# Performance work log

Measured on AMD Instinct MI355X. Metric: run time of the kernel, lower is better.

The kernel has to match this reference:

```python
import jax, jax.numpy as jnp
import numpy as np

D = 128
EMB = 1024
B, S = 4, 4096


def setup_inputs() -> dict:
    key = jax.random.key(0)
    ks = jax.random.split(key, 7)
    scale = 1.0 / np.sqrt(EMB)
    return {
        "X": jax.random.normal(ks[0], (B, S, EMB), dtype=jnp.float32),
        "lam": jnp.float32(0.8),
        "Wq": jax.random.uniform(ks[1], (EMB, 2 * D), jnp.float32, -scale, scale),
        "bq": jax.random.uniform(ks[2], (2 * D,), jnp.float32, -scale, scale),
        "Wk": jax.random.uniform(ks[3], (EMB, 2 * D), jnp.float32, -scale, scale),
        "bk": jax.random.uniform(ks[4], (2 * D,), jnp.float32, -scale, scale),
        "Wv": jax.random.uniform(ks[5], (EMB, D), jnp.float32, -scale, scale),
        "bv": jax.random.uniform(ks[6], (D,), jnp.float32, -scale, scale),
    }


def reference(X, lam, Wq, bq, Wk, bk, Wv, bv):
    # Projections: Q,K are [B,S,2d]; V is [B,S,d]
    Q = X @ Wq + bq
    K = X @ Wk + bk
    V = X @ Wv + bv
    Q1, Q2 = Q[..., :D], Q[..., D:]
    K1, K2 = K[..., :D], K[..., D:]
    s = 1.0 / jnp.sqrt(jnp.float32(D))
    # Dual QK^T scores [B,S,S]
    A1 = jnp.einsum("bqd,bkd->bqk", Q1, K1) * s
    A2 = jnp.einsum("bqd,bkd->bqk", Q2, K2) * s
    P = jax.nn.softmax(A1, axis=-1) - lam * jax.nn.softmax(A2, axis=-1)
    return jnp.einsum("bqk,bkd->bqd", P, V)
```

## Files before the change

### kernel.cpp

```cpp
#include <hip/hip_runtime.h>
#include <hip/hip_bf16.h>


typedef __attribute__((ext_vector_type(8))) short bf16x8;
typedef __attribute__((ext_vector_type(4))) float f32x4;
typedef __attribute__((ext_vector_type(16))) float f32x16;

#define MFMA16(a, b, c) __builtin_amdgcn_mfma_f32_16x16x32_bf16((a), (b), (c), 0, 0, 0)
#define MFMA32(a, b, c) __builtin_amdgcn_mfma_f32_32x32x16_bf16((a), (b), (c), 0, 0, 0)

__device__ __forceinline__ unsigned short f2bf(float x) {
    union { float f; unsigned u; } v; v.f = x;
    return (unsigned short)((v.u + 0x7FFFu + ((v.u >> 16) & 1u)) >> 16);
}
__device__ __forceinline__ unsigned pk2bf(float a, float b) {
    __hip_bfloat162 h = __float22bfloat162_rn(float2{a, b});
    union { __hip_bfloat162 h2; unsigned u; } cv; cv.h2 = h;
    return cv.u;
}
__device__ __forceinline__ float fexp2(float x) {
    float r; asm("v_exp_f32 %0, %1" : "=v"(r) : "v"(x)); return r;
}

__global__ __launch_bounds__(256) void wtrans_kernel(
    const float* __restrict__ Wq, const float* __restrict__ Wk,
    const float* __restrict__ Wv, unsigned short* __restrict__ Wt) {
    int tid = blockIdx.x * 256 + threadIdx.x;
    int k = tid & 1023, n = tid >> 10;
    float v;
    if (n < 256)      v = Wq[k * 256 + n];
    else if (n < 512) v = Wk[k * 256 + (n - 256)];
    else              v = Wv[k * 128 + (n - 512)];
    Wt[tid] = f2bf(v);
}

__global__ __launch_bounds__(256) void proj_kernel(
    const float* __restrict__ X, const unsigned short* __restrict__ Wt,
    const float* __restrict__ bq, const float* __restrict__ bk,
    const float* __restrict__ bv,
    unsigned short* __restrict__ Qs, unsigned short* __restrict__ Kb,
    unsigned short* __restrict__ Vb) {
    __shared__ alignas(16) char lds[16384];
    const int nt = blockIdx.y;
    const int m0 = blockIdx.x * 128;
    const int t = threadIdx.x, w = t >> 6, l = t & 63, c = l & 15, g = l >> 4;
    const int wm = w >> 1, wn = w & 1;
    const unsigned short* Wrow = Wt + (long)(nt * 128) * 1024;

    f32x4 acc[4][4];
    const f32x4 fz = {0.f, 0.f, 0.f, 0.f};
#pragma unroll
    for (int i = 0; i < 4; i++)
#pragma unroll
        for (int j = 0; j < 4; j++) acc[i][j] = fz;

    const int srow = t >> 1, sh = t & 1;
    const int sswz = (srow & 7) << 4;
    for (int k0 = 0; k0 < 1024; k0 += 32) {
        const float* xs = X + (long)(m0 + srow) * 1024 + k0 + sh * 16;
        float4 f0 = *(const float4*)(xs + 0);
        float4 f1 = *(const float4*)(xs + 4);
        float4 f2 = *(const float4*)(xs + 8);
        float4 f3 = *(const float4*)(xs + 12);
        const unsigned short* wsc = Wrow + (long)srow * 1024 + k0 + sh * 16;
        uint4 w0 = *(const uint4*)(wsc + 0);
        uint4 w1 = *(const uint4*)(wsc + 8);
        uint4 xa, xb;
        xa.x = pk2bf(f0.x, f0.y); xa.y = pk2bf(f0.z, f0.w);
        xa.z = pk2bf(f1.x, f1.y); xa.w = pk2bf(f1.z, f1.w);
        xb.x = pk2bf(f2.x, f2.y); xb.y = pk2bf(f2.z, f2.w);
        xb.z = pk2bf(f3.x, f3.y); xb.w = pk2bf(f3.z, f3.w);
        int base = srow * 64 + sh * 32;
        *(uint4*)(lds + ((base + 0) ^ sswz)) = xa;
        *(uint4*)(lds + ((base + 16) ^ sswz)) = xb;
        *(uint4*)(lds + 8192 + ((base + 0) ^ sswz)) = w0;
        *(uint4*)(lds + 8192 + ((base + 16) ^ sswz)) = w1;
        __syncthreads();

        bf16x8 af[4];
#pragma unroll
        for (int am = 0; am < 4; am++) {
            int r_ = wm * 64 + am * 16 + c;
            af[am] = *(const bf16x8*)(lds + ((r_ * 64 + g * 16) ^ ((c & 7) << 4)));
        }
#pragma unroll
        for (int bn = 0; bn < 4; bn++) {
            int r_ = wn * 64 + bn * 16 + c;
            bf16x8 bfr = *(const bf16x8*)(lds + 8192 + ((r_ * 64 + g * 16) ^ ((c & 7) << 4)));
#pragma unroll
            for (int am = 0; am < 4; am++) acc[am][bn] = MFMA16(af[am], bfr, acc[am][bn]);
        }
        __syncthreads();
    }

    const float QSCALE = 0.08838834764831845f * 1.4426950408889634f;
    const float* bias; float scale; unsigned short* outp; int ostride, ocol0, boff;
    if (nt < 2)      { bias = bq; boff = nt * 128;       scale = QSCALE; outp = Qs; ostride = 256; ocol0 = nt * 128; }
    else if (nt < 4) { bias = bk; boff = (nt - 2) * 128; scale = 1.0f;   outp = Kb; ostride = 256; ocol0 = (nt - 2) * 128; }
    else             { bias = bv; boff = 0;              scale = 1.0f;   outp = Vb; ostride = 128; ocol0 = 0; }
#pragma unroll
    for (int bn = 0; bn < 4; bn++) {
        int ncol = wn * 64 + bn * 16 + c;
        float bb = bias[boff + ncol];
#pragma unroll
        for (int am = 0; am < 4; am++) {
#pragma unroll
            for (int r = 0; r < 4; r++) {
                long row = m0 + wm * 64 + am * 16 + 4 * g + r;
                outp[row * ostride + ocol0 + ncol] = f2bf((acc[am][bn][r] + bb) * scale);
            }
        }
    }
}

__global__ __launch_bounds__(256) void vtrans_kernel(
    const unsigned short* __restrict__ Vb, unsigned short* __restrict__ Vt) {
    int tid = blockIdx.x * 256 + threadIdx.x;
    int s = tid & 4095, d = (tid >> 12) & 127, b = tid >> 19;
    Vt[tid] = Vb[(((long)b << 12) + s) * 128 + d];
}

__global__ __launch_bounds__(512) void attn2_kernel(
    const unsigned short* __restrict__ Qs, const unsigned short* __restrict__ Kb,
    const unsigned short* __restrict__ Vt,
    float* __restrict__ Po, float* __restrict__ Ps, int nsplit, int ks) {
    __shared__ alignas(16) char lds[49152];
    const int t = threadIdx.x;
    const int w = t >> 6, l = t & 63, r31 = l & 31, hi = l >> 5;
    const int wq = w >> 1, br = w & 1;

    const int total = gridDim.x;
    const int lin = (blockIdx.x & 7) * (total >> 3) + (blockIdx.x >> 3);
    const int grp = lin >> 5, qb = lin & 31;
    const int b = grp / nsplit, split = grp % nsplit;

    const long qrow = (long)b * 4096 + qb * 128 + wq * 32 + r31;
    bf16x8 qf[8];
    const unsigned short* Qp = Qs + qrow * 256 + br * 128 + hi * 8;
#pragma unroll
    for (int ds = 0; ds < 8; ds++) qf[ds] = *(const bf16x8*)(Qp + ds * 16);

    f32x16 o[4];
    const f32x16 oz = {};
#pragma unroll
    for (int dt = 0; dt < 4; dt++) o[dt] = oz;
    float m = -1e30f, s = 0.f;

    const int krow = t >> 4, kseg = t & 15, khalf = kseg >> 3;
    const int kdoff = khalf * 8192 + (((krow * 256 + (kseg & 7) * 32)) ^
                                      (((krow & 7) << 4) ^ (khalf << 5)));
    const int vrow = t >> 2, vq = t & 3;
    const unsigned short* vsrc = Vt + (((long)b * 128 + vrow) << 12);
    const int voff = 16384 + ((vrow * 64 + vq * 16) ^ ((vrow & 7) << 4));
    const long kbb = (long)b * 4096;

    const int kb0 = split * ks, kend = kb0 + ks;
    uint4 kr0, kr1, vr0;
#define LOADTILE(KN)                                                        \
    {                                                                       \
        const unsigned short* kp = Kb + (kbb + (KN) + krow) * 256 + kseg * 16; \
        kr0 = *(const uint4*)(kp);                                          \
        kr1 = *(const uint4*)(kp + 8);                                      \
        vr0 = *(const uint4*)(vsrc + (KN) + vq * 8);                        \
    }
#define WRITETILE(BUF)                                                      \
    {                                                                       \
        char* bb_ = lds + (BUF)*24576;                                      \
        *(uint4*)(bb_ + kdoff) = kr0;                                       \
        *(uint4*)(bb_ + (kdoff ^ 16)) = kr1;                                \
        *(uint4*)(bb_ + voff) = vr0;                                        \
    }

    LOADTILE(kb0);
    WRITETILE(0);
    {
        int kn = (kb0 + 32 < kend) ? kb0 + 32 : kb0;
        LOADTILE(kn);
    }

    const int krd_sw = ((r31 & 7) << 4) ^ (br << 5);
    const int kbofs = br * 8192;
    int cur = 0;

    for (int kb = kb0; kb < kend; kb += 32) {
        __syncthreads();
        if (kb + 32 < kend) {
            WRITETILE(cur ^ 1);
            int kn = (kb + 64 < kend) ? kb + 64 : kb0;
            LOADTILE(kn);
        }
        const char* bufp = lds + cur * 24576;
        const char* kbase = bufp + kbofs;

        f32x16 pa = oz, pb_ = oz;
#pragma unroll
        for (int ds = 0; ds < 4; ds++) {
            bf16x8 kfa = *(const bf16x8*)(kbase + ((r31 * 256 + ds * 32 + hi * 16) ^ krd_sw));
            bf16x8 kfb = *(const bf16x8*)(kbase + ((r31 * 256 + (ds + 4) * 32 + hi * 16) ^ krd_sw));
            pa = MFMA32(kfa, qf[ds], pa);
            pb_ = MFMA32(kfb, qf[ds + 4], pb_);
        }
        f32x16 p;
#pragma unroll
        for (int i = 0; i < 16; i++) p[i] = pa[i] + pb_[i];

        float x0 = fmaxf(fmaxf(p[0], p[1]), fmaxf(p[2], p[3]));
        float x1 = fmaxf(fmaxf(p[4], p[5]), fmaxf(p[6], p[7]));
        float x2 = fmaxf(fmaxf(p[8], p[9]), fmaxf(p[10], p[11]));
        float x3 = fmaxf(fmaxf(p[12], p[13]), fmaxf(p[14], p[15]));
        float lmx = fmaxf(fmaxf(x0, x1), fmaxf(x2, x3));
        lmx = fmaxf(lmx, __shfl_xor(lmx, 32));
        if (__any(lmx > m + 8.f)) {
            float mn = fmaxf(m, lmx);
            float al = fexp2(m - mn);
            s *= al; m = mn;
#pragma unroll
            for (int dt = 0; dt < 4; dt++) o[dt] *= al;
        }
        float pe[16];
#pragma unroll
        for (int i = 0; i < 16; i++) pe[i] = fexp2(p[i] - m);
        float s0 = (pe[0] + pe[1]) + (pe[2] + pe[3]);
        float s1 = (pe[4] + pe[5]) + (pe[6] + pe[7]);
        float s2 = (pe[8] + pe[9]) + (pe[10] + pe[11]);
        float s3 = (pe[12] + pe[13]) + (pe[14] + pe[15]);
        float ps_ = (s0 + s1) + (s2 + s3);
        ps_ += __shfl_xor(ps_, 32);
        s += ps_;

        unsigned cA = pk2bf(pe[0], pe[1]), cB = pk2bf(pe[2], pe[3]);
        unsigned cC = pk2bf(pe[4], pe[5]), cD = pk2bf(pe[6], pe[7]);
        asm volatile("v_permlane32_swap_b32 %0, %1" : "+v"(cA), "+v"(cC));
        asm volatile("v_permlane32_swap_b32 %0, %1" : "+v"(cB), "+v"(cD));
        unsigned dA = pk2bf(pe[8], pe[9]), dB = pk2bf(pe[10], pe[11]);
        unsigned dC = pk2bf(pe[12], pe[13]), dD = pk2bf(pe[14], pe[15]);
        asm volatile("v_permlane32_swap_b32 %0, %1" : "+v"(dA), "+v"(dC));
        asm volatile("v_permlane32_swap_b32 %0, %1" : "+v"(dB), "+v"(dD));
        union { uint4 u; bf16x8 v; } pb0, pb1;
        pb0.u = uint4{cA, cB, cC, cD};
        pb1.u = uint4{dA, dB, dC, dD};

#pragma unroll
        for (int dt = 0; dt < 4; dt++) {
            int vr = dt * 32 + r31;
            int vsw = (vr & 7) << 4;
            bf16x8 vf0 = *(const bf16x8*)(bufp + 16384 + ((vr * 64 + hi * 16) ^ vsw));
            bf16x8 vf1 = *(const bf16x8*)(bufp + 16384 + ((vr * 64 + 32 + hi * 16) ^ vsw));
            o[dt] = MFMA32(vf0, pb0.v, o[dt]);
            o[dt] = MFMA32(vf1, pb1.v, o[dt]);
        }
        cur ^= 1;
    }

    float* po = Po + (((qrow)*nsplit + split) * 2 + br) * 128;
#pragma unroll
    for (int dt = 0; dt < 4; dt++) {
#pragma unroll
        for (int rg = 0; rg < 4; rg++) {
            float4 v;
            v.x = o[dt][rg * 4 + 0];
            v.y = o[dt][rg * 4 + 1];
            v.z = o[dt][rg * 4 + 2];
            v.w = o[dt][rg * 4 + 3];
            *(float4*)(po + dt * 32 + rg * 8 + hi * 4) = v;
        }
    }
    if (hi == 0)
        *(float2*)(Ps + (qrow * nsplit + split) * 4 + br * 2) = float2{m, s};
}

__global__ __launch_bounds__(256) void combine_kernel(
    const float* __restrict__ Po, const float* __restrict__ Ps,
    const float* __restrict__ lam_p, float* __restrict__ out, int nsplit) {
    int tid = blockIdx.x * 256 + threadIdx.x;
    int q = tid >> 5, dq = (tid & 31) * 4;
    float M1 = -1e30f, M2 = -1e30f;
    for (int s = 0; s < nsplit; s++) {
        float4 st = *(const float4*)(Ps + (long)(q * nsplit + s) * 4);
        M1 = fmaxf(M1, st.x); M2 = fmaxf(M2, st.z);
    }
    float S1 = 0.f, S2 = 0.f;
    float a0 = 0.f, a1 = 0.f, a2 = 0.f, a3 = 0.f;
    float b0 = 0.f, b1 = 0.f, b2 = 0.f, b3 = 0.f;
    for (int s = 0; s < nsplit; s++) {
        float4 st = *(const float4*)(Ps + (long)(q * nsplit + s) * 4);
        float w1 = fexp2(st.x - M1), w2 = fexp2(st.z - M2);
        S1 += st.y * w1; S2 += st.w * w2;
        const float* p1 = Po + (((long)q * nsplit + s) * 2 + 0) * 128 + dq;
        const float* p2 = Po + (((long)q * nsplit + s) * 2 + 1) * 128 + dq;
        float4 v1 = *(const float4*)p1;
        float4 v2 = *(const float4*)p2;
        a0 += v1.x * w1; a1 += v1.y * w1; a2 += v1.z * w1; a3 += v1.w * w1;
        b0 += v2.x * w2; b1 += v2.y * w2; b2 += v2.z * w2; b3 += v2.w * w2;
    }
    float lam = *lam_p;
    float i1 = 1.f / S1, i2 = lam / S2;
    float4 v;
    v.x = a0 * i1 - b0 * i2;
    v.y = a1 * i1 - b1 * i2;
    v.z = a2 * i1 - b2 * i2;
    v.w = a3 * i1 - b3 * i2;
    *(float4*)(out + (long)q * 128 + dq) = v;
}

extern "C" void kernel_launch(void* const* d_in, const int* in_sizes, int n_in,
                              void* d_out, int out_size, void* d_ws, size_t ws_size,
                              hipStream_t stream) {
    const float* X   = (const float*)d_in[0];
    const float* lam = (const float*)d_in[1];
    const float* Wq  = (const float*)d_in[2];
    const float* bq  = (const float*)d_in[3];
    const float* Wk  = (const float*)d_in[4];
    const float* bk  = (const float*)d_in[5];
    const float* Wv  = (const float*)d_in[6];
    const float* bv  = (const float*)d_in[7];
    char* ws = (char*)d_ws;
    unsigned short* Qs = (unsigned short*)(ws);
    unsigned short* Kb = (unsigned short*)(ws + (8u << 20));
    unsigned short* Vb = (unsigned short*)(ws + (16u << 20));
    unsigned short* Vt = (unsigned short*)(ws + (20u << 20));
    unsigned short* Wt = (unsigned short*)(ws + (24u << 20));
    const size_t base = (size_t)26 << 20;
    const size_t NQ = 16384;
    int nsplit = 1;
    if (ws_size >= base + NQ * 4 * 2 * 128 * 4 + NQ * 4 * 4 * 4)      nsplit = 4;
    else if (ws_size >= base + NQ * 2 * 2 * 128 * 4 + NQ * 2 * 4 * 4) nsplit = 2;
    float* Po = (float*)(ws + base);
    float* Ps = (float*)(ws + base + NQ * (size_t)nsplit * 2 * 128 * 4);

    wtrans_kernel<<<2560, 256, 0, stream>>>(Wq, Wk, Wv, Wt);
    proj_kernel<<<dim3(128, 5), 256, 0, stream>>>(X, Wt, bq, bk, bv, Qs, Kb, Vb);
    vtrans_kernel<<<8192, 256, 0, stream>>>(Vb, Vt);
    attn2_kernel<<<128 * nsplit, 512, 0, stream>>>(Qs, Kb, Vt, Po, Ps,
                                                   nsplit, 4096 / nsplit);
    combine_kernel<<<2048, 256, 0, stream>>>(Po, Ps, lam, (float*)d_out, nsplit);
}
```

Before: 172.6 us.

## Fuse V transpose into projection epilogue and halve attention block size

The projection kernel now writes V directly in transposed layout, which removes the separate vtrans kernel launch and its global round-trip. The attention kernel moves from 512-thread, 128-query blocks to 256-thread, 64-query blocks with twice as many blocks. Each thread loads more per tile, LDS swizzles are replaced by precomputed rotation offsets, and s_setprio is raised around the MFMA sections. The V epilogue stores are strided scatter writes, and the smaller blocks reload K/V tiles more often per query.

```diff
diff --git a/kernel.cpp b/kernel.cpp
--- a/kernel.cpp
+++ b/kernel.cpp
@@ -39,7 +39,7 @@
     const float* __restrict__ bq, const float* __restrict__ bk,
     const float* __restrict__ bv,
     unsigned short* __restrict__ Qs, unsigned short* __restrict__ Kb,
-    unsigned short* __restrict__ Vb) {
+    unsigned short* __restrict__ Vt) {
     __shared__ alignas(16) char lds[16384];
     const int nt = blockIdx.y;
     const int m0 = blockIdx.x * 128;
@@ -94,33 +94,42 @@
     }
 
     const float QSCALE = 0.08838834764831845f * 1.4426950408889634f;
-    const float* bias; float scale; unsigned short* outp; int ostride, ocol0, boff;
-    if (nt < 2)      { bias = bq; boff = nt * 128;       scale = QSCALE; outp = Qs; ostride = 256; ocol0 = nt * 128; }
-    else if (nt < 4) { bias = bk; boff = (nt - 2) * 128; scale = 1.0f;   outp = Kb; ostride = 256; ocol0 = (nt - 2) * 128; }
-    else             { bias = bv; boff = 0;              scale = 1.0f;   outp = Vb; ostride = 128; ocol0 = 0; }
-#pragma unroll
-    for (int bn = 0; bn < 4; bn++) {
-        int ncol = wn * 64 + bn * 16 + c;
-        float bb = bias[boff + ncol];
-#pragma unroll
-        for (int am = 0; am < 4; am++) {
-#pragma unroll
-            for (int r = 0; r < 4; r++) {
-                long row = m0 + wm * 64 + am * 16 + 4 * g + r;
-                outp[row * ostride + ocol0 + ncol] = f2bf((acc[am][bn][r] + bb) * scale);
+    if (nt < 4) {
+        const float* bias; float scale; unsigned short* outp; int ocol0, boff;
+        if (nt < 2) { bias = bq; boff = nt * 128;       scale = QSCALE; outp = Qs; ocol0 = nt * 128; }
+        else        { bias = bk; boff = (nt - 2) * 128; scale = 1.0f;   outp = Kb; ocol0 = (nt - 2) * 128; }
+#pragma unroll
+        for (int bn = 0; bn < 4; bn++) {
+            int ncol = wn * 64 + bn * 16 + c;
+            float bb = bias[boff + ncol];
+#pragma unroll
+            for (int am = 0; am < 4; am++) {
+#pragma unroll
+                for (int r = 0; r < 4; r++) {
+                    long row = m0 + wm * 64 + am * 16 + 4 * g + r;
+                    outp[row * 256 + ocol0 + ncol] = f2bf((acc[am][bn][r] + bb) * scale);
+                }
             }
         }
-    }
-}
-
-__global__ __launch_bounds__(256) void vtrans_kernel(
-    const unsigned short* __restrict__ Vb, unsigned short* __restrict__ Vt) {
-    int tid = blockIdx.x * 256 + threadIdx.x;
-    int s = tid & 4095, d = (tid >> 12) & 127, b = tid >> 19;
-    Vt[tid] = Vb[(((long)b << 12) + s) * 128 + d];
-}
-
-__global__ __launch_bounds__(512) void attn2_kernel(
+    } else {
+#pragma unroll
+        for (int bn = 0; bn < 4; bn++) {
+            int ncol = wn * 64 + bn * 16 + c;
+            float bb = bv[ncol];
+            unsigned short* vcol = Vt + ((long)((m0 >> 12) * 128 + ncol) << 12);
+#pragma unroll
+            for (int am = 0; am < 4; am++) {
+#pragma unroll
+                for (int r = 0; r < 4; r++) {
+                    int ss = (m0 & 4095) + wm * 64 + am * 16 + 4 * g + r;
+                    vcol[ss] = f2bf(acc[am][bn][r] + bb);
+                }
+            }
+        }
+    }
+}
+
+__global__ __launch_bounds__(256) void attn2_kernel(
     const unsigned short* __restrict__ Qs, const unsigned short* __restrict__ Kb,
     const unsigned short* __restrict__ Vt,
     float* __restrict__ Po, float* __restrict__ Ps, int nsplit, int ks) {
@@ -131,10 +140,10 @@
 
     const int total = gridDim.x;
     const int lin = (blockIdx.x & 7) * (total >> 3) + (blockIdx.x >> 3);
-    const int grp = lin >> 5, qb = lin & 31;
+    const int grp = lin >> 6, qb = lin & 63;
     const int b = grp / nsplit, split = grp % nsplit;
 
-    const long qrow = (long)b * 4096 + qb * 128 + wq * 32 + r31;
+    const long qrow = (long)b * 4096 + qb * 64 + wq * 32 + r31;
     bf16x8 qf[8];
     const unsigned short* Qp = Qs + qrow * 256 + br * 128 + hi * 8;
 #pragma unroll
@@ -146,29 +155,54 @@
     for (int dt = 0; dt < 4; dt++) o[dt] = oz;
     float m = -1e30f, s = 0.f;
 
-    const int krow = t >> 4, kseg = t & 15, khalf = kseg >> 3;
-    const int kdoff = khalf * 8192 + (((krow * 256 + (kseg & 7) * 32)) ^
-                                      (((krow & 7) << 4) ^ (khalf << 5)));
-    const int vrow = t >> 2, vq = t & 3;
-    const unsigned short* vsrc = Vt + (((long)b * 128 + vrow) << 12);
-    const int voff = 16384 + ((vrow * 64 + vq * 16) ^ ((vrow & 7) << 4));
+    const int krow = t >> 3, kseg = t & 7;
+    const int khalf = kseg >> 2, kcb = (kseg & 3) * 64;
+    int kw[4];
+#pragma unroll
+    for (int j = 0; j < 4; j++)
+        kw[j] = khalf * 8192 + krow * 256 + ((kcb + j * 16 + (krow << 4)) & 255);
+    const int vrow = t >> 1, vhalf = t & 1;
+    int vw[2];
+#pragma unroll
+    for (int j = 0; j < 2; j++)
+        vw[j] = 16384 + vrow * 64 + ((vhalf * 32 + j * 16 + ((vrow >> 1) << 4)) & 63);
+    const unsigned short* vsrc = Vt + (((long)b * 128 + vrow) << 12) + vhalf * 16;
     const long kbb = (long)b * 4096;
 
     const int kb0 = split * ks, kend = kb0 + ks;
-    uint4 kr0, kr1, vr0;
-#define LOADTILE(KN)                                                        \
-    {                                                                       \
-        const unsigned short* kp = Kb + (kbb + (KN) + krow) * 256 + kseg * 16; \
-        kr0 = *(const uint4*)(kp);                                          \
-        kr1 = *(const uint4*)(kp + 8);                                      \
-        vr0 = *(const uint4*)(vsrc + (KN) + vq * 8);                        \
-    }
-#define WRITETILE(BUF)                                                      \
-    {                                                                       \
-        char* bb_ = lds + (BUF)*24576;                                      \
-        *(uint4*)(bb_ + kdoff) = kr0;                                       \
-        *(uint4*)(bb_ + (kdoff ^ 16)) = kr1;                                \
-        *(uint4*)(bb_ + voff) = vr0;                                        \
+    uint4 kA, kB, kC, kD, vA, vB;
+#define LOADTILE(KN)                                                           \
+    {                                                                          \
+        const unsigned short* kp = Kb + (kbb + (KN) + krow) * 256 + kseg * 32; \
+        kA = *(const uint4*)(kp);                                              \
+        kB = *(const uint4*)(kp + 8);                                          \
+        kC = *(const uint4*)(kp + 16);                                         \
+        kD = *(const uint4*)(kp + 24);                                         \
+        const unsigned short* vp = vsrc + (KN);                                \
+        vA = *(const uint4*)(vp);                                              \
+        vB = *(const uint4*)(vp + 8);                                          \
+    }
+#define WRITETILE(BUF)                                                         \
+    {                                                                          \
+        char* bb_ = lds + (BUF)*24576;                                         \
+        *(uint4*)(bb_ + kw[0]) = kA;                                           \
+        *(uint4*)(bb_ + kw[1]) = kB;                                           \
+        *(uint4*)(bb_ + kw[2]) = kC;                                           \
+        *(uint4*)(bb_ + kw[3]) = kD;                                           \
+        *(uint4*)(bb_ + vw[0]) = vA;                                           \
+        *(uint4*)(bb_ + vw[1]) = vB;                                           \
+    }
+
+    int kro[8];
+#pragma unroll
+    for (int ds = 0; ds < 8; ds++)
+        kro[ds] = br * 8192 + r31 * 256 + ((ds * 32 + hi * 16 + (r31 << 4)) & 255);
+    int vro0[4], vro1[4];
+#pragma unroll
+    for (int dt = 0; dt < 4; dt++) {
+        int vr = dt * 32 + r31;
+        vro0[dt] = 16384 + vr * 64 + ((hi * 16 + ((vr >> 1) << 4)) & 63);
+        vro1[dt] = 16384 + vr * 64 + ((32 + hi * 16 + ((vr >> 1) << 4)) & 63);
     }
 
     LOADTILE(kb0);
@@ -177,9 +211,6 @@
         int kn = (kb0 + 32 < kend) ? kb0 + 32 : kb0;
         LOADTILE(kn);
     }
-
-    const int krd_sw = ((r31 & 7) << 4) ^ (br << 5);
-    const int kbofs = br * 8192;
     int cur = 0;
 
     for (int kb = kb0; kb < kend; kb += 32) {
@@ -190,16 +221,17 @@
             LOADTILE(kn);
         }
         const char* bufp = lds + cur * 24576;
-        const char* kbase = bufp + kbofs;
 
         f32x16 pa = oz, pb_ = oz;
+        __builtin_amdgcn_s_setprio(1);
 #pragma unroll
         for (int ds = 0; ds < 4; ds++) {
-            bf16x8 kfa = *(const bf16x8*)(kbase + ((r31 * 256 + ds * 32 + hi * 16) ^ krd_sw));
-            bf16x8 kfb = *(const bf16x8*)(kbase + ((r31 * 256 + (ds + 4) * 32 + hi * 16) ^ krd_sw));
+            bf16x8 kfa = *(const bf16x8*)(bufp + kro[ds]);
+            bf16x8 kfb = *(const bf16x8*)(bufp + kro[ds + 4]);
             pa = MFMA32(kfa, qf[ds], pa);
             pb_ = MFMA32(kfb, qf[ds + 4], pb_);
         }
+        __builtin_amdgcn_s_setprio(0);
         f32x16 p;
 #pragma unroll
         for (int i = 0; i < 16; i++) p[i] = pa[i] + pb_[i];
@@ -240,19 +272,19 @@
         pb0.u = uint4{cA, cB, cC, cD};
         pb1.u = uint4{dA, dB, dC, dD};
 
+        __builtin_amdgcn_s_setprio(1);
 #pragma unroll
         for (int dt = 0; dt < 4; dt++) {
-            int vr = dt * 32 + r31;
-            int vsw = (vr & 7) << 4;
-            bf16x8 vf0 = *(const bf16x8*)(bufp + 16384 + ((vr * 64 + hi * 16) ^ vsw));
-            bf16x8 vf1 = *(const bf16x8*)(bufp + 16384 + ((vr * 64 + 32 + hi * 16) ^ vsw));
+            bf16x8 vf0 = *(const bf16x8*)(bufp + vro0[dt]);
+            bf16x8 vf1 = *(const bf16x8*)(bufp + vro1[dt]);
             o[dt] = MFMA32(vf0, pb0.v, o[dt]);
             o[dt] = MFMA32(vf1, pb1.v, o[dt]);
         }
+        __builtin_amdgcn_s_setprio(0);
         cur ^= 1;
     }
 
-    float* po = Po + (((qrow)*nsplit + split) * 2 + br) * 128;
+    float* po = Po + ((qrow * nsplit + split) * 2 + br) * 128;
 #pragma unroll
     for (int dt = 0; dt < 4; dt++) {
 #pragma unroll
@@ -317,21 +349,18 @@
     char* ws = (char*)d_ws;
     unsigned short* Qs = (unsigned short*)(ws);
     unsigned short* Kb = (unsigned short*)(ws + (8u << 20));
-    unsigned short* Vb = (unsigned short*)(ws + (16u << 20));
-    unsigned short* Vt = (unsigned short*)(ws + (20u << 20));
-    unsigned short* Wt = (unsigned short*)(ws + (24u << 20));
-    const size_t base = (size_t)26 << 20;
-    const size_t NQ = 16384;
+    unsigned short* Vt = (unsigned short*)(ws + (16u << 20));
+    unsigned short* Wt = (unsigned short*)(ws + (20u << 20));
+    const size_t base = (size_t)22 << 20;
     int nsplit = 1;
-    if (ws_size >= base + NQ * 4 * 2 * 128 * 4 + NQ * 4 * 4 * 4)      nsplit = 4;
-    else if (ws_size >= base + NQ * 2 * 2 * 128 * 4 + NQ * 2 * 4 * 4) nsplit = 2;
+    if (ws_size >= base + 4u * (16777216u + 262144u))      nsplit = 4;
+    else if (ws_size >= base + 2u * (16777216u + 262144u)) nsplit = 2;
     float* Po = (float*)(ws + base);
-    float* Ps = (float*)(ws + base + NQ * (size_t)nsplit * 2 * 128 * 4);
+    float* Ps = (float*)(ws + base + (size_t)16777216 * nsplit);
 
     wtrans_kernel<<<2560, 256, 0, stream>>>(Wq, Wk, Wv, Wt);
-    proj_kernel<<<dim3(128, 5), 256, 0, stream>>>(X, Wt, bq, bk, bv, Qs, Kb, Vb);
-    vtrans_kernel<<<8192, 256, 0, stream>>>(Vb, Vt);
-    attn2_kernel<<<128 * nsplit, 512, 0, stream>>>(Qs, Kb, Vt, Po, Ps,
+    proj_kernel<<<dim3(128, 5), 256, 0, stream>>>(X, Wt, bq, bk, bv, Qs, Kb, Vt);
+    attn2_kernel<<<256 * nsplit, 256, 0, stream>>>(Qs, Kb, Vt, Po, Ps,
                                                    nsplit, 4096 / nsplit);
     combine_kernel<<<2048, 256, 0, stream>>>(Po, Ps, lam, (float*)d_out, nsplit);
 }
```

After: 267.2 us. +54.8%, slower.

## Stream K/V tiles via direct global-to-LDS loads with 4-stage ring buffer

Applied to the files above, without the earlier changes.

Replaces the register-staged double buffer in the attention kernel with global_load_lds direct copies into a 4-deep LDS ring, issuing loads three tiles ahead and using vmcnt waits plus a raw barrier. The XOR swizzle becomes a rotation applied on the source address so that direct LDS writes stay conflict-free, and the read offsets are precomputed. It also raises wave priority around the MFMA blocks. This removes VGPR staging and the LDS store instructions, at the cost of doubling LDS to 96KB, which may limit occupancy to one block per CU.

```diff
diff --git a/kernel.cpp b/kernel.cpp
--- a/kernel.cpp
+++ b/kernel.cpp
@@ -8,6 +8,10 @@
 
 #define MFMA16(a, b, c) __builtin_amdgcn_mfma_f32_16x16x32_bf16((a), (b), (c), 0, 0, 0)
 #define MFMA32(a, b, c) __builtin_amdgcn_mfma_f32_32x32x16_bf16((a), (b), (c), 0, 0, 0)
+
+typedef const __attribute__((address_space(1))) void gas_void;
+typedef __attribute__((address_space(3))) void las_void;
+#define GLOAD16(G, L) __builtin_amdgcn_global_load_lds((gas_void*)(G), (las_void*)(L), 16, 0, 0)
 
 __device__ __forceinline__ unsigned short f2bf(float x) {
     union { float f; unsigned u; } v; v.f = x;
@@ -120,11 +124,11 @@
     Vt[tid] = Vb[(((long)b << 12) + s) * 128 + d];
 }
 
-__global__ __launch_bounds__(512) void attn2_kernel(
+__global__ __launch_bounds__(512) void attn3_kernel(
     const unsigned short* __restrict__ Qs, const unsigned short* __restrict__ Kb,
     const unsigned short* __restrict__ Vt,
     float* __restrict__ Po, float* __restrict__ Ps, int nsplit, int ks) {
-    __shared__ alignas(16) char lds[49152];
+    __shared__ alignas(16) char lds[98304];
     const int t = threadIdx.x;
     const int w = t >> 6, l = t & 63, r31 = l & 31, hi = l >> 5;
     const int wq = w >> 1, br = w & 1;
@@ -146,60 +150,68 @@
     for (int dt = 0; dt < 4; dt++) o[dt] = oz;
     float m = -1e30f, s = 0.f;
 
-    const int krow = t >> 4, kseg = t & 15, khalf = kseg >> 3;
-    const int kdoff = khalf * 8192 + (((krow * 256 + (kseg & 7) * 32)) ^
-                                      (((krow & 7) << 4) ^ (khalf << 5)));
-    const int vrow = t >> 2, vq = t & 3;
-    const unsigned short* vsrc = Vt + (((long)b * 128 + vrow) << 12);
-    const int voff = 16384 + ((vrow * 64 + vq * 16) ^ ((vrow & 7) << 4));
+    const int krow = w * 4 + (l >> 4);
+    const int kc = (l & 15) * 16;
+    const int ksrc_rot = (kc - krow * 16) & 255;
+    const int vd = w * 16 + (l >> 2);
+    const int vc = (l & 3) * 16;
     const long kbb = (long)b * 4096;
+    const char* KbB = (const char*)Kb;
+    const char* VtB = (const char*)Vt + ((long)b * 128 + vd) * 8192 +
+                      ((vc - ((vd >> 1) & 3) * 16) & 63);
+    char* dst0 = lds + w * 1024;
 
     const int kb0 = split * ks, kend = kb0 + ks;
-    uint4 kr0, kr1, vr0;
-#define LOADTILE(KN)                                                        \
-    {                                                                       \
-        const unsigned short* kp = Kb + (kbb + (KN) + krow) * 256 + kseg * 16; \
-        kr0 = *(const uint4*)(kp);                                          \
-        kr1 = *(const uint4*)(kp + 8);                                      \
-        vr0 = *(const uint4*)(vsrc + (KN) + vq * 8);                        \
-    }
-#define WRITETILE(BUF)                                                      \
-    {                                                                       \
-        char* bb_ = lds + (BUF)*24576;                                      \
-        *(uint4*)(bb_ + kdoff) = kr0;                                       \
-        *(uint4*)(bb_ + (kdoff ^ 16)) = kr1;                                \
-        *(uint4*)(bb_ + voff) = vr0;                                        \
-    }
-
-    LOADTILE(kb0);
-    WRITETILE(0);
-    {
-        int kn = (kb0 + 32 < kend) ? kb0 + 32 : kb0;
-        LOADTILE(kn);
-    }
-
-    const int krd_sw = ((r31 & 7) << 4) ^ (br << 5);
-    const int kbofs = br * 8192;
+#define STAGE(KB_, BUF_)                                                       \
+    {                                                                          \
+        const char* s1_ = KbB + (kbb + (KB_) + krow) * 512 + ksrc_rot;         \
+        char* d_ = dst0 + (BUF_)*24576;                                        \
+        GLOAD16(s1_, d_);                                                      \
+        GLOAD16(s1_ + 256, d_ + 8192);                                         \
+        GLOAD16(VtB + (long)(KB_)*2, d_ + 16384);                              \
+    }
+
+    int kro[8];
+#pragma unroll
+    for (int ds = 0; ds < 8; ds++)
+        kro[ds] = br * 8192 + r31 * 256 + ((ds * 32 + hi * 16 + r31 * 16) & 255);
+    int vro0[4], vro1[4];
+#pragma unroll
+    for (int dt = 0; dt < 4; dt++) {
+        int vr = dt * 32 + r31, rot = ((vr >> 1) & 3) * 16;
+        vro0[dt] = 16384 + vr * 64 + ((hi * 16 + rot) & 63);
+        vro1[dt] = 16384 + vr * 64 + ((32 + hi * 16 + rot) & 63);
+    }
+
+    STAGE(kb0, 0);
+    STAGE(kb0 + 32, 1);
+    STAGE(kb0 + 64, 2);
     int cur = 0;
 
     for (int kb = kb0; kb < kend; kb += 32) {
-        __syncthreads();
-        if (kb + 32 < kend) {
-            WRITETILE(cur ^ 1);
-            int kn = (kb + 64 < kend) ? kb + 64 : kb0;
-            LOADTILE(kn);
+        asm volatile("s_waitcnt vmcnt(6)" ::: "memory");
+        __builtin_amdgcn_sched_barrier(0);
+        __builtin_amdgcn_s_barrier();
+        asm volatile("" ::: "memory");
+        __builtin_amdgcn_sched_barrier(0);
+
+        {
+            int kn = kb + 96;
+            if (kn >= kend) kn = kb0;
+            STAGE(kn, (cur + 3) & 3);
         }
         const char* bufp = lds + cur * 24576;
-        const char* kbase = bufp + kbofs;
 
         f32x16 pa = oz, pb_ = oz;
+        __builtin_amdgcn_s_setprio(1);
 #pragma unroll
         for (int ds = 0; ds < 4; ds++) {
-            bf16x8 kfa = *(const bf16x8*)(kbase + ((r31 * 256 + ds * 32 + hi * 16) ^ krd_sw));
-            bf16x8 kfb = *(const bf16x8*)(kbase + ((r31 * 256 + (ds + 4) * 32 + hi * 16) ^ krd_sw));
+            bf16x8 kfa = *(const bf16x8*)(bufp + kro[ds]);
+            bf16x8 kfb = *(const bf16x8*)(bufp + kro[ds + 4]);
             pa = MFMA32(kfa, qf[ds], pa);
             pb_ = MFMA32(kfb, qf[ds + 4], pb_);
         }
+        __builtin_amdgcn_s_setprio(0);
         f32x16 p;
 #pragma unroll
         for (int i = 0; i < 16; i++) p[i] = pa[i] + pb_[i];
@@ -240,19 +252,19 @@
         pb0.u = uint4{cA, cB, cC, cD};
         pb1.u = uint4{dA, dB, dC, dD};
 
+        __builtin_amdgcn_s_setprio(1);
 #pragma unroll
         for (int dt = 0; dt < 4; dt++) {
-            int vr = dt * 32 + r31;
-            int vsw = (vr & 7) << 4;
-            bf16x8 vf0 = *(const bf16x8*)(bufp + 16384 + ((vr * 64 + hi * 16) ^ vsw));
-            bf16x8 vf1 = *(const bf16x8*)(bufp + 16384 + ((vr * 64 + 32 + hi * 16) ^ vsw));
+            bf16x8 vf0 = *(const bf16x8*)(bufp + vro0[dt]);
+            bf16x8 vf1 = *(const bf16x8*)(bufp + vro1[dt]);
             o[dt] = MFMA32(vf0, pb0.v, o[dt]);
             o[dt] = MFMA32(vf1, pb1.v, o[dt]);
         }
-        cur ^= 1;
-    }
-
-    float* po = Po + (((qrow)*nsplit + split) * 2 + br) * 128;
+        __builtin_amdgcn_s_setprio(0);
+        cur = (cur + 1) & 3;
+    }
+
+    float* po = Po + ((qrow * nsplit + split) * 2 + br) * 128;
 #pragma unroll
     for (int dt = 0; dt < 4; dt++) {
 #pragma unroll
@@ -331,7 +343,7 @@
     wtrans_kernel<<<2560, 256, 0, stream>>>(Wq, Wk, Wv, Wt);
     proj_kernel<<<dim3(128, 5), 256, 0, stream>>>(X, Wt, bq, bk, bv, Qs, Kb, Vb);
     vtrans_kernel<<<8192, 256, 0, stream>>>(Vb, Vt);
-    attn2_kernel<<<128 * nsplit, 512, 0, stream>>>(Qs, Kb, Vt, Po, Ps,
+    attn3_kernel<<<128 * nsplit, 512, 0, stream>>>(Qs, Kb, Vt, Po, Ps,
                                                    nsplit, 4096 / nsplit);
     combine_kernel<<<2048, 256, 0, stream>>>(Po, Ps, lam, (float*)d_out, nsplit);
 }
```

New measurement: 174.9 us. Within noise of the previous version (+1.4%).
